# Optimization experiments

Hardware: AMD Instinct MI355X
Metric: run time of the kernel (lower is better)

The kernel has to match this reference:

```python
import jax, jax.numpy as jnp
from jax import lax
import numpy as np

DG = 2          # deformable groups
KH = KW = 3     # kernel size
KK = KH * KW
PAD = 1


def setup_inputs() -> dict:
    key = jax.random.key(0)
    k1, k2, k3 = jax.random.split(key, 3)
    B, C, H, W = 4, 64, 128, 128
    O = 64
    x = jax.random.normal(k1, (B, C, H, W), jnp.float32)
    # original inits offset weights to 0 (degenerate: plain conv); use small random
    # weights instead so the irregular bilinear-gather path is actually exercised.
    w_off = jax.random.normal(k2, (DG * 2 * KK, C, KH, KW), jnp.float32) * 0.05
    w_def = jax.random.normal(k3, (O, C, KH, KW), jnp.float32) * (1.0 / np.sqrt(C * KK))
    return {"x": x, "w_off": w_off, "w_def": w_def}


def _deform_conv(x, w_off, w_def):
    B, C, H, W = x.shape
    O = w_def.shape[0]
    Cg = C // DG

    # offset = offset_conv(x): stride 1, pad 1, no bias -> [B, DG*2*KK, H, W]
    offset = lax.conv_general_dilated(
        x, w_off, window_strides=(1, 1), padding=((PAD, PAD), (PAD, PAD)),
        dimension_numbers=("NCHW", "OIHW", "NCHW"))
    # DCN layout: per group, per kernel tap k, channel 2k = dy, 2k+1 = dx
    off = offset.reshape(B, DG, KK, 2, H, W)

    ki, kj = jnp.meshgrid(jnp.arange(KH), jnp.arange(KW), indexing="ij")
    ki = (ki.reshape(KK) - PAD).astype(x.dtype)   # kernel row offsets -1..1
    kj = (kj.reshape(KK) - PAD).astype(x.dtype)
    hh = jnp.arange(H, dtype=x.dtype)
    ww = jnp.arange(W, dtype=x.dtype)

    # sampling positions [B, DG, KK, H, W]
    py = off[:, :, :, 0] + ki[None, None, :, None, None] + hh[None, None, None, :, None]
    px = off[:, :, :, 1] + kj[None, None, :, None, None] + ww[None, None, None, None, :]

    y0 = jnp.floor(py).astype(jnp.int32)
    x0 = jnp.floor(px).astype(jnp.int32)
    dy = py - y0.astype(x.dtype)
    dx = px - x0.astype(x.dtype)

    x_g = x.reshape(B, DG, Cg, H * W)

    def gather(yi, xi):
        # zero padding outside the image
        valid = ((yi >= 0) & (yi < H) & (xi >= 0) & (xi < W)).astype(x.dtype)
        yc = jnp.clip(yi, 0, H - 1)
        xc = jnp.clip(xi, 0, W - 1)
        idx = (yc * W + xc).reshape(B, DG, 1, KK * H * W)
        v = jnp.take_along_axis(x_g, idx, axis=3).reshape(B, DG, Cg, KK, H, W)
        return v * valid[:, :, None]  # broadcast over channel axis

    # bilinear interpolation at learned offset positions
    val = (gather(y0, x0) * ((1 - dy) * (1 - dx))[:, :, None]
           + gather(y0, x0 + 1) * ((1 - dy) * dx)[:, :, None]
           + gather(y0 + 1, x0) * (dy * (1 - dx))[:, :, None]
           + gather(y0 + 1, x0 + 1) * (dy * dx)[:, :, None])

    # weighted accumulation: conv groups = 1, channel dim = DG*Cg
    w = w_def.reshape(O, DG, Cg, KK)
    return jnp.einsum("bgckhw,ogck->bohw", val, w)


def reference(x, w_off, w_def):
    return _deform_conv(x, w_off, w_def)
```

## Files before the change

### kernel.cpp

```cpp
#include <hip/hip_runtime.h>
#include <hip/hip_bf16.h>

typedef short bf16x8 __attribute__((ext_vector_type(8)));
typedef float f32x4  __attribute__((ext_vector_type(4)));

#define Bn 4
#define Cn 64
#define Hn 128
#define Wn 128
#define HWn 16384

#define XT_BYTES    (Bn*HWn*Cn*2)
#define PKDEF_BYTES (18*4*64*8*2)

static __device__ __forceinline__ unsigned pk_bf16(float lo, float hi) {
  union { __hip_bfloat162 h; unsigned u; } cv;
  cv.h = __float22bfloat162_rn(make_float2(lo, hi));
  return cv.u;
}
static __device__ __forceinline__ float blo(unsigned u) { return __uint_as_float(u << 16); }
static __device__ __forceinline__ float bhi(unsigned u) { return __uint_as_float(u & 0xffff0000u); }

__global__ __launch_bounds__(256) void transpose_cast(const float* __restrict__ x,
                                                      ushort* __restrict__ xt) {
  __shared__ float tile[64][65];
  const int t = threadIdx.x;
  const int blk = blockIdx.x;
  const int b = blk >> 8;
  const int pix0 = (blk & 255) * 64;
  const int y = pix0 >> 7, x0 = pix0 & 127;
  const float* xb = x + (b * Cn) * HWn + pix0;
#pragma unroll
  for (int q = 0; q < 16; ++q) {
    int idx = q * 256 + t;
    int c = idx >> 6, p = idx & 63;
    tile[c][p] = xb[c * HWn + p];
  }
  __syncthreads();
  const int p = t & 63, cg = t >> 6;
#pragma unroll
  for (int half = 0; half < 2; ++half) {
    const int seg = cg * 2 + half;
    unsigned u[4];
#pragma unroll
    for (int j = 0; j < 4; ++j)
      u[j] = pk_bf16(tile[seg * 8 + 2 * j][p], tile[seg * 8 + 2 * j + 1][p]);
    uint4 v = {u[0], u[1], u[2], u[3]};
    *(uint4*)(xt + (((((b << 7) + y) << 3) + seg) * 128 + x0 + p) * 8) = v;
  }
}

__global__ __launch_bounds__(256) void prep_pack(const float* __restrict__ w_off,
                                                 const float* __restrict__ w_def,
                                                 ushort* __restrict__ pk_def,
                                                 ushort* __restrict__ pk_off) {
  const int t = blockIdx.x * 256 + threadIdx.x;
  if (t < 4608) {
    int lane = t & 63, oc = (t >> 6) & 3, s = t >> 8;
    int g = s / 9, k = s % 9;
    int o = oc * 16 + (lane & 15);
    int cb = g * 32 + (lane >> 4) * 8;
    unsigned u[4];
#pragma unroll
    for (int j = 0; j < 4; ++j)
      u[j] = pk_bf16(w_def[(o * Cn + cb + 2 * j) * 9 + k],
                     w_def[(o * Cn + cb + 2 * j + 1) * 9 + k]);
    uint4 v = {u[0], u[1], u[2], u[3]};
    *(uint4*)(pk_def + t * 8) = v;
  } else if (t < 8064) {
    int t2 = t - 4608;
    int lane = t2 & 63, r = t2 >> 6;
    int oc = r % 3, s = r / 3;
    int k = s >> 1, chalf = s & 1;
    int o = oc * 16 + (lane & 15);
    int cb = chalf * 32 + (lane >> 4) * 8;
    unsigned u[4];
#pragma unroll
    for (int j = 0; j < 4; ++j) {
      float lo = (o < 36) ? w_off[(o * Cn + cb + 2 * j) * 9 + k] : 0.f;
      float hi = (o < 36) ? w_off[(o * Cn + cb + 2 * j + 1) * 9 + k] : 0.f;
      u[j] = pk_bf16(lo, hi);
    }
    uint4 v = {u[0], u[1], u[2], u[3]};
    *(uint4*)(pk_off + (r * 64 + lane) * 8) = v;
  }
}

__global__ __launch_bounds__(512, 4) void deform_fused(const ushort* __restrict__ xt,
                                                       const ushort* __restrict__ pk_def,
                                                       const ushort* __restrict__ pk_off,
                                                       float* __restrict__ out) {
  __shared__ ushort tile[13 * 25 * 72];
  __shared__ float off_lds[4][36][17];
  const int lane = threadIdx.x & 63;
  const int wid = threadIdx.x >> 6;
  const int pg = wid >> 1, gsel = wid & 1;
  int bid = blockIdx.x;
  bid = (bid & 7) * 128 + (bid >> 3);
  const int b  = bid >> 8;
  const int ty = (bid >> 3) & 31;
  const int tx = bid & 7;
  const int y0t = ty * 4, x0t = tx * 16;
  const int TLY = max(0, y0t - 4), THY = min(127, y0t + 8);
  const int TLX = max(0, x0t - 4), THX = min(127, x0t + 20);
  const int Hd = THY - TLY + 1, Wd = THX - TLX + 1;

  {
    const int xq = threadIdx.x & 31;
    const int r0 = threadIdx.x >> 5;
    const int nr = Hd * 8;
    for (int rr = r0; rr < nr; rr += 16) {
      const int yq = rr >> 3, seg = rr & 7;
      if (xq < Wd) {
        const ushort* src = xt + ((((b << 7) + TLY + yq) << 3) + seg) * 1024 + (TLX + xq) * 8;
        *(uint4*)&tile[(yq * 25 + xq) * 72 + seg * 8] = *(const uint4*)src;
      }
    }
  }
  __syncthreads();

  const int h = y0t + pg;
  const int p = lane & 15, kq = lane >> 4;
  const int w_ = x0t + p;
  const int pixin = (h << 7) + x0t;
  const int su = gsel * 4 + kq;
  const int colb = lane & 15;

  {
    f32x4 oa0 = {0,0,0,0}, oa1 = {0,0,0,0}, oa2 = {0,0,0,0};
    const bf16x8* pBo = (const bf16x8*)pk_off;
#pragma unroll
    for (int s = 0; s < 18; ++s) {
      const int k = s >> 1, chalf = s & 1;
      int y = h + k / 3 - 1, xx = w_ + k % 3 - 1;
      bool valid = ((unsigned)y < 128u) && ((unsigned)xx < 128u);
      int yc = min(max(y, 0), 127), xc = min(max(xx, 0), 127);
      const int seg = chalf * 4 + kq;
      uint4 t_ = *(const uint4*)&tile[((yc - TLY) * 25 + (xc - TLX)) * 72 + seg * 8];
      if (!valid) { t_.x = 0; t_.y = 0; t_.z = 0; t_.w = 0; }
      union { uint4 u; bf16x8 v; } A; A.u = t_;
      if (gsel == 0) {
        oa0 = __builtin_amdgcn_mfma_f32_16x16x32_bf16(A.v, pBo[(s*3 + 0)*64 + lane], oa0, 0,0,0);
        oa2 = __builtin_amdgcn_mfma_f32_16x16x32_bf16(A.v, pBo[(s*3 + 2)*64 + lane], oa2, 0,0,0);
      } else {
        oa1 = __builtin_amdgcn_mfma_f32_16x16x32_bf16(A.v, pBo[(s*3 + 1)*64 + lane], oa1, 0,0,0);
      }
    }
    if (gsel == 0) {
#pragma unroll
      for (int r = 0; r < 4; ++r) {
        off_lds[pg][colb][kq * 4 + r] = oa0[r];
        if (colb < 4) off_lds[pg][32 + colb][kq * 4 + r] = oa2[r];
      }
    } else {
#pragma unroll
      for (int r = 0; r < 4; ++r) off_lds[pg][16 + colb][kq * 4 + r] = oa1[r];
    }
  }
  __syncthreads();

  float offv[18];
#pragma unroll
  for (int j = 0; j < 18; ++j) offv[j] = off_lds[pg][gsel * 18 + j][p];

  f32x4 acc0={0,0,0,0}, acc1={0,0,0,0}, acc2={0,0,0,0}, acc3={0,0,0,0};
  const bf16x8* pB = (const bf16x8*)pk_def;

#pragma unroll
  for (int j = 0; j < 9; ++j) {
    const int k = j;
    float py = offv[2*j]   + (float)(h  + k / 3 - 1);
    float px = offv[2*j+1] + (float)(w_ + k % 3 - 1);
    float fy = floorf(py), fx = floorf(px);
    int y0 = (int)fy, x0 = (int)fx;
    float dy = py - fy, dx = px - fx;

    bool vy0 = (y0 >= 0) && (y0 < Hn);
    bool vy1 = (y0 >= -1) && (y0 < Hn - 1);
    bool vx0 = (x0 >= 0) && (x0 < Wn);
    bool vx1 = (x0 >= -1) && (x0 < Wn - 1);
    float omdy = 1.f - dy, omdx = 1.f - dx;
    float w00 = (vy0 && vx0) ? omdy * omdx : 0.f;
    float w01 = (vy0 && vx1) ? omdy * dx   : 0.f;
    float w10 = (vy1 && vx0) ? dy * omdx   : 0.f;
    float w11 = (vy1 && vx1) ? dy * dx     : 0.f;

    int iy0 = min(max(y0, 0), Hn - 1), iy1 = min(max(y0 + 1, 0), Hn - 1);
    int ix0 = min(max(x0, 0), Wn - 1), ix1 = min(max(x0 + 1, 0), Wn - 1);

    uint4 c00, c01, c10, c11;
    bool intile = (iy0 >= TLY) && (iy1 <= THY) && (ix0 >= TLX) && (ix1 <= THX);
    if (__all((int)intile)) {
      const int ly0 = iy0 - TLY, ly1 = iy1 - TLY;
      const int lx0 = ix0 - TLX, lx1 = ix1 - TLX;
      c00 = *(const uint4*)&tile[(ly0 * 25 + lx0) * 72 + su * 8];
      c01 = *(const uint4*)&tile[(ly0 * 25 + lx1) * 72 + su * 8];
      c10 = *(const uint4*)&tile[(ly1 * 25 + lx0) * 72 + su * 8];
      c11 = *(const uint4*)&tile[(ly1 * 25 + lx1) * 72 + su * 8];
    } else {
      const int r0g = ((((b << 7) + iy0) << 3) + su) * 128;
      const int r1g = ((((b << 7) + iy1) << 3) + su) * 128;
      c00 = *(const uint4*)(xt + (r0g + ix0) * 8);
      c01 = *(const uint4*)(xt + (r0g + ix1) * 8);
      c10 = *(const uint4*)(xt + (r1g + ix0) * 8);
      c11 = *(const uint4*)(xt + (r1g + ix1) * 8);
    }

    unsigned au[4];
#define BILC(comp, idx)                                                        \
    { float l = w00 * blo(c00.comp); l = fmaf(w01, blo(c01.comp), l);          \
      l = fmaf(w10, blo(c10.comp), l); l = fmaf(w11, blo(c11.comp), l);        \
      float hh = w00 * bhi(c00.comp); hh = fmaf(w01, bhi(c01.comp), hh);       \
      hh = fmaf(w10, bhi(c10.comp), hh); hh = fmaf(w11, bhi(c11.comp), hh);    \
      au[idx] = pk_bf16(l, hh); }
    BILC(x, 0) BILC(y, 1) BILC(z, 2) BILC(w, 3)
#undef BILC
    union { uint4 u; bf16x8 v; } A;
    A.u.x = au[0]; A.u.y = au[1]; A.u.z = au[2]; A.u.w = au[3];

    const int s = gsel * 9 + j;
    acc0 = __builtin_amdgcn_mfma_f32_16x16x32_bf16(A.v, pB[(s*4 + 0)*64 + lane], acc0, 0,0,0);
    acc1 = __builtin_amdgcn_mfma_f32_16x16x32_bf16(A.v, pB[(s*4 + 1)*64 + lane], acc1, 0,0,0);
    acc2 = __builtin_amdgcn_mfma_f32_16x16x32_bf16(A.v, pB[(s*4 + 2)*64 + lane], acc2, 0,0,0);
    acc3 = __builtin_amdgcn_mfma_f32_16x16x32_bf16(A.v, pB[(s*4 + 3)*64 + lane], acc3, 0,0,0);
  }

  __syncthreads();
  float* red = (float*)tile;
  if (gsel == 1) {
    *(f32x4*)&red[((pg * 4 + 0) * 64 + lane) * 4] = acc0;
    *(f32x4*)&red[((pg * 4 + 1) * 64 + lane) * 4] = acc1;
    *(f32x4*)&red[((pg * 4 + 2) * 64 + lane) * 4] = acc2;
    *(f32x4*)&red[((pg * 4 + 3) * 64 + lane) * 4] = acc3;
  }
  __syncthreads();
  if (gsel == 0) {
    acc0 += *(const f32x4*)&red[((pg * 4 + 0) * 64 + lane) * 4];
    acc1 += *(const f32x4*)&red[((pg * 4 + 1) * 64 + lane) * 4];
    acc2 += *(const f32x4*)&red[((pg * 4 + 2) * 64 + lane) * 4];
    acc3 += *(const f32x4*)&red[((pg * 4 + 3) * 64 + lane) * 4];
    float* ob = out + pixin + kq * 4;
#pragma unroll
    for (int r = 0; r < 4; ++r) {
      ob[((b*64 +      colb) << 14) + r] = acc0[r];
      ob[((b*64 + 16 + colb) << 14) + r] = acc1[r];
      ob[((b*64 + 32 + colb) << 14) + r] = acc2[r];
      ob[((b*64 + 48 + colb) << 14) + r] = acc3[r];
    }
  }
}

extern "C" void kernel_launch(void* const* d_in, const int* in_sizes, int n_in,
                              void* d_out, int out_size, void* d_ws, size_t ws_size,
                              hipStream_t stream) {
  const float* x     = (const float*)d_in[0];
  const float* w_off = (const float*)d_in[1];
  const float* w_def = (const float*)d_in[2];
  float* out = (float*)d_out;

  char* ws = (char*)d_ws;
  ushort* xt     = (ushort*)ws;
  ushort* pk_def = (ushort*)(ws + XT_BYTES);
  ushort* pk_off = (ushort*)(ws + XT_BYTES + PKDEF_BYTES);

  transpose_cast<<<1024, 256, 0, stream>>>(x, xt);
  prep_pack<<<32, 256, 0, stream>>>(w_off, w_def, pk_def, pk_off);
  deform_fused<<<1024, 512, 0, stream>>>(xt, pk_def, pk_off, out);
}
```

Before: 54.42 us.

## Switch to fp16 with packed-half bilinear math, shrink halo tile, raise occupancy

Converts the transposed input and packed weights from bf16 to fp16 and uses f16 MFMA. The bilinear interpolation now runs in packed half2 arithmetic instead of unpacking to fp32 and repacking, which cuts VALU work in the gather loop. The LDS tile halo is narrowed from 25 to 23 columns and the launch-bounds occupancy hint goes from 4 to 6 blocks, so more blocks can fit per CU. The offset-conv MFMA work is also rebalanced between the two wave groups. The risks are fp16 range and precision loss in the interpolation, more samples falling outside the narrower tile onto the global fallback path, and register pressure from the higher occupancy target.

```diff
diff --git a/kernel.cpp b/kernel.cpp
--- a/kernel.cpp
+++ b/kernel.cpp
@@ -1,7 +1,8 @@
 #include <hip/hip_runtime.h>
 #include <hip/hip_bf16.h>
 
-typedef short bf16x8 __attribute__((ext_vector_type(8)));
+typedef _Float16 f16x8 __attribute__((ext_vector_type(8)));
+typedef _Float16 f16x2 __attribute__((ext_vector_type(2)));
 typedef float f32x4  __attribute__((ext_vector_type(4)));
 
 #define Bn 4
@@ -13,13 +14,11 @@
 #define XT_BYTES    (Bn*HWn*Cn*2)
 #define PKDEF_BYTES (18*4*64*8*2)
 
-static __device__ __forceinline__ unsigned pk_bf16(float lo, float hi) {
-  union { __hip_bfloat162 h; unsigned u; } cv;
-  cv.h = __float22bfloat162_rn(make_float2(lo, hi));
+static __device__ __forceinline__ unsigned pk_f16(float lo, float hi) {
+  union { _Float16 h[2]; unsigned u; } cv;
+  cv.h[0] = (_Float16)lo; cv.h[1] = (_Float16)hi;
   return cv.u;
 }
-static __device__ __forceinline__ float blo(unsigned u) { return __uint_as_float(u << 16); }
-static __device__ __forceinline__ float bhi(unsigned u) { return __uint_as_float(u & 0xffff0000u); }
 
 __global__ __launch_bounds__(256) void transpose_cast(const float* __restrict__ x,
                                                       ushort* __restrict__ xt) {
@@ -44,7 +43,7 @@
     unsigned u[4];
 #pragma unroll
     for (int j = 0; j < 4; ++j)
-      u[j] = pk_bf16(tile[seg * 8 + 2 * j][p], tile[seg * 8 + 2 * j + 1][p]);
+      u[j] = pk_f16(tile[seg * 8 + 2 * j][p], tile[seg * 8 + 2 * j + 1][p]);
     uint4 v = {u[0], u[1], u[2], u[3]};
     *(uint4*)(xt + (((((b << 7) + y) << 3) + seg) * 128 + x0 + p) * 8) = v;
   }
@@ -63,8 +62,8 @@
     unsigned u[4];
 #pragma unroll
     for (int j = 0; j < 4; ++j)
-      u[j] = pk_bf16(w_def[(o * Cn + cb + 2 * j) * 9 + k],
-                     w_def[(o * Cn + cb + 2 * j + 1) * 9 + k]);
+      u[j] = pk_f16(w_def[(o * Cn + cb + 2 * j) * 9 + k],
+                    w_def[(o * Cn + cb + 2 * j + 1) * 9 + k]);
     uint4 v = {u[0], u[1], u[2], u[3]};
     *(uint4*)(pk_def + t * 8) = v;
   } else if (t < 8064) {
@@ -79,18 +78,18 @@
     for (int j = 0; j < 4; ++j) {
       float lo = (o < 36) ? w_off[(o * Cn + cb + 2 * j) * 9 + k] : 0.f;
       float hi = (o < 36) ? w_off[(o * Cn + cb + 2 * j + 1) * 9 + k] : 0.f;
-      u[j] = pk_bf16(lo, hi);
+      u[j] = pk_f16(lo, hi);
     }
     uint4 v = {u[0], u[1], u[2], u[3]};
     *(uint4*)(pk_off + (r * 64 + lane) * 8) = v;
   }
 }
 
-__global__ __launch_bounds__(512, 4) void deform_fused(const ushort* __restrict__ xt,
+__global__ __launch_bounds__(512, 6) void deform_fused(const ushort* __restrict__ xt,
                                                        const ushort* __restrict__ pk_def,
                                                        const ushort* __restrict__ pk_off,
                                                        float* __restrict__ out) {
-  __shared__ ushort tile[13 * 25 * 72];
+  __shared__ ushort tile[13 * 23 * 72];
   __shared__ float off_lds[4][36][17];
   const int lane = threadIdx.x & 63;
   const int wid = threadIdx.x >> 6;
@@ -102,7 +101,7 @@
   const int tx = bid & 7;
   const int y0t = ty * 4, x0t = tx * 16;
   const int TLY = max(0, y0t - 4), THY = min(127, y0t + 8);
-  const int TLX = max(0, x0t - 4), THX = min(127, x0t + 20);
+  const int TLX = max(0, x0t - 3), THX = min(127, x0t + 19);
   const int Hd = THY - TLY + 1, Wd = THX - TLX + 1;
 
   {
@@ -113,7 +112,7 @@
       const int yq = rr >> 3, seg = rr & 7;
       if (xq < Wd) {
         const ushort* src = xt + ((((b << 7) + TLY + yq) << 3) + seg) * 1024 + (TLX + xq) * 8;
-        *(uint4*)&tile[(yq * 25 + xq) * 72 + seg * 8] = *(const uint4*)src;
+        *(uint4*)&tile[(yq * 23 + xq) * 72 + seg * 8] = *(const uint4*)src;
       }
     }
   }
@@ -128,7 +127,7 @@
 
   {
     f32x4 oa0 = {0,0,0,0}, oa1 = {0,0,0,0}, oa2 = {0,0,0,0};
-    const bf16x8* pBo = (const bf16x8*)pk_off;
+    const f16x8* pBo = (const f16x8*)pk_off;
 #pragma unroll
     for (int s = 0; s < 18; ++s) {
       const int k = s >> 1, chalf = s & 1;
@@ -136,25 +135,25 @@
       bool valid = ((unsigned)y < 128u) && ((unsigned)xx < 128u);
       int yc = min(max(y, 0), 127), xc = min(max(xx, 0), 127);
       const int seg = chalf * 4 + kq;
-      uint4 t_ = *(const uint4*)&tile[((yc - TLY) * 25 + (xc - TLX)) * 72 + seg * 8];
+      uint4 t_ = *(const uint4*)&tile[((yc - TLY) * 23 + (xc - TLX)) * 72 + seg * 8];
       if (!valid) { t_.x = 0; t_.y = 0; t_.z = 0; t_.w = 0; }
-      union { uint4 u; bf16x8 v; } A; A.u = t_;
+      union { uint4 u; f16x8 v; } A; A.u = t_;
       if (gsel == 0) {
-        oa0 = __builtin_amdgcn_mfma_f32_16x16x32_bf16(A.v, pBo[(s*3 + 0)*64 + lane], oa0, 0,0,0);
-        oa2 = __builtin_amdgcn_mfma_f32_16x16x32_bf16(A.v, pBo[(s*3 + 2)*64 + lane], oa2, 0,0,0);
+        oa0 = __builtin_amdgcn_mfma_f32_16x16x32_f16(A.v, pBo[(s*3 + 0)*64 + lane], oa0, 0,0,0);
       } else {
-        oa1 = __builtin_amdgcn_mfma_f32_16x16x32_bf16(A.v, pBo[(s*3 + 1)*64 + lane], oa1, 0,0,0);
+        oa1 = __builtin_amdgcn_mfma_f32_16x16x32_f16(A.v, pBo[(s*3 + 1)*64 + lane], oa1, 0,0,0);
+        oa2 = __builtin_amdgcn_mfma_f32_16x16x32_f16(A.v, pBo[(s*3 + 2)*64 + lane], oa2, 0,0,0);
       }
     }
     if (gsel == 0) {
 #pragma unroll
+      for (int r = 0; r < 4; ++r) off_lds[pg][colb][kq * 4 + r] = oa0[r];
+    } else {
+#pragma unroll
       for (int r = 0; r < 4; ++r) {
-        off_lds[pg][colb][kq * 4 + r] = oa0[r];
+        off_lds[pg][16 + colb][kq * 4 + r] = oa1[r];
         if (colb < 4) off_lds[pg][32 + colb][kq * 4 + r] = oa2[r];
       }
-    } else {
-#pragma unroll
-      for (int r = 0; r < 4; ++r) off_lds[pg][16 + colb][kq * 4 + r] = oa1[r];
     }
   }
   __syncthreads();
@@ -164,7 +163,7 @@
   for (int j = 0; j < 18; ++j) offv[j] = off_lds[pg][gsel * 18 + j][p];
 
   f32x4 acc0={0,0,0,0}, acc1={0,0,0,0}, acc2={0,0,0,0}, acc3={0,0,0,0};
-  const bf16x8* pB = (const bf16x8*)pk_def;
+  const f16x8* pB = (const f16x8*)pk_def;
 
 #pragma unroll
   for (int j = 0; j < 9; ++j) {
@@ -193,10 +192,10 @@
     if (__all((int)intile)) {
       const int ly0 = iy0 - TLY, ly1 = iy1 - TLY;
       const int lx0 = ix0 - TLX, lx1 = ix1 - TLX;
-      c00 = *(const uint4*)&tile[(ly0 * 25 + lx0) * 72 + su * 8];
-      c01 = *(const uint4*)&tile[(ly0 * 25 + lx1) * 72 + su * 8];
-      c10 = *(const uint4*)&tile[(ly1 * 25 + lx0) * 72 + su * 8];
-      c11 = *(const uint4*)&tile[(ly1 * 25 + lx1) * 72 + su * 8];
+      c00 = *(const uint4*)&tile[(ly0 * 23 + lx0) * 72 + su * 8];
+      c01 = *(const uint4*)&tile[(ly0 * 23 + lx1) * 72 + su * 8];
+      c10 = *(const uint4*)&tile[(ly1 * 23 + lx0) * 72 + su * 8];
+      c11 = *(const uint4*)&tile[(ly1 * 23 + lx1) * 72 + su * 8];
     } else {
       const int r0g = ((((b << 7) + iy0) << 3) + su) * 128;
       const int r1g = ((((b << 7) + iy1) << 3) + su) * 128;
@@ -206,23 +205,25 @@
       c11 = *(const uint4*)(xt + (r1g + ix1) * 8);
     }
 
-    unsigned au[4];
-#define BILC(comp, idx)                                                        \
-    { float l = w00 * blo(c00.comp); l = fmaf(w01, blo(c01.comp), l);          \
-      l = fmaf(w10, blo(c10.comp), l); l = fmaf(w11, blo(c11.comp), l);        \
-      float hh = w00 * bhi(c00.comp); hh = fmaf(w01, bhi(c01.comp), hh);       \
-      hh = fmaf(w10, bhi(c10.comp), hh); hh = fmaf(w11, bhi(c11.comp), hh);    \
-      au[idx] = pk_bf16(l, hh); }
-    BILC(x, 0) BILC(y, 1) BILC(z, 2) BILC(w, 3)
+    const _Float16 h00 = (_Float16)w00, h01 = (_Float16)w01;
+    const _Float16 h10 = (_Float16)w10, h11 = (_Float16)w11;
+    const f16x2 W00 = {h00, h00}, W01 = {h01, h01};
+    const f16x2 W10 = {h10, h10}, W11 = {h11, h11};
+    union U32H { unsigned u; f16x2 h; };
+    union { uint4 u; f16x8 v; } A;
+#define BILC(comp, fld)                                                        \
+    { U32H a0, a1, a2, a3, r;                                                  \
+      a0.u = c00.comp; a1.u = c01.comp; a2.u = c10.comp; a3.u = c11.comp;      \
+      r.h = a0.h * W00 + a1.h * W01 + a2.h * W10 + a3.h * W11;                 \
+      A.u.fld = r.u; }
+    BILC(x, x) BILC(y, y) BILC(z, z) BILC(w, w)
 #undef BILC
-    union { uint4 u; bf16x8 v; } A;
-    A.u.x = au[0]; A.u.y = au[1]; A.u.z = au[2]; A.u.w = au[3];
 
     const int s = gsel * 9 + j;
-    acc0 = __builtin_amdgcn_mfma_f32_16x16x32_bf16(A.v, pB[(s*4 + 0)*64 + lane], acc0, 0,0,0);
-    acc1 = __builtin_amdgcn_mfma_f32_16x16x32_bf16(A.v, pB[(s*4 + 1)*64 + lane], acc1, 0,0,0);
-    acc2 = __builtin_amdgcn_mfma_f32_16x16x32_bf16(A.v, pB[(s*4 + 2)*64 + lane], acc2, 0,0,0);
-    acc3 = __builtin_amdgcn_mfma_f32_16x16x32_bf16(A.v, pB[(s*4 + 3)*64 + lane], acc3, 0,0,0);
+    acc0 = __builtin_amdgcn_mfma_f32_16x16x32_f16(A.v, pB[(s*4 + 0)*64 + lane], acc0, 0,0,0);
+    acc1 = __builtin_amdgcn_mfma_f32_16x16x32_f16(A.v, pB[(s*4 + 1)*64 + lane], acc1, 0,0,0);
+    acc2 = __builtin_amdgcn_mfma_f32_16x16x32_f16(A.v, pB[(s*4 + 2)*64 + lane], acc2, 0,0,0);
+    acc3 = __builtin_amdgcn_mfma_f32_16x16x32_f16(A.v, pB[(s*4 + 3)*64 + lane], acc3, 0,0,0);
   }
 
   __syncthreads();
```

Result: no change. 53.70 us (-1.3%).
